# Optimization experiments

Measured on AMD Instinct MI355X. Metric: run time of the kernel, lower is better.

## Reference

```python
import jax, jax.numpy as jnp
import numpy as np

B, S, H, D = 8, 1024, 8, 64      # batch, seq_len, num_heads, num_hidden
DM = H * D                        # input model dim = 512
DK = 64.0                         # d_k scale
EPS = 1e-3                        # keras GroupNormalization default epsilon


def setup_inputs() -> dict:
    key = jax.random.key(0)
    ks = jax.random.split(key, 12)
    sc = 1.0 / np.sqrt(DM)
    return {
        "query":  jax.random.normal(ks[0], (B, S, DM), jnp.float32),
        "key":    jax.random.normal(ks[1], (B, S, DM), jnp.float32),
        "values": jax.random.normal(ks[2], (B, S, DM), jnp.float32),
        "Wq": jax.random.normal(ks[3], (DM, 3 * H * D), jnp.float32) * sc,
        "bq": jnp.zeros((3 * H * D,), jnp.float32),
        "Wk": jax.random.normal(ks[4], (DM, 2 * H * D), jnp.float32) * sc,
        "bk": jnp.zeros((2 * H * D,), jnp.float32),
        "Wv": jax.random.normal(ks[5], (DM, H * D), jnp.float32) * sc,
        "bv": jnp.zeros((H * D,), jnp.float32),
        "gamma": jnp.ones((D,), jnp.float32),
        "beta": jnp.zeros((D,), jnp.float32),
        "lam": jax.random.uniform(ks[6], (1,), jnp.float32),          # trainable lambda
        "lambda_init": jax.random.uniform(ks[7], (1,), jnp.float32),  # frozen lambda_init
    }


def reference(query, key, values, Wq, bq, Wk, bk, Wv, bv, gamma, beta, lam, lambda_init):
    # projections -> (B, H, S, *)
    q = (query @ Wq + bq).reshape(B, S, H, 3 * D).transpose(0, 2, 1, 3)
    k = (key @ Wk + bk).reshape(B, S, H, 2 * D).transpose(0, 2, 1, 3)
    v = (values @ Wv + bv).reshape(B, S, H, D).transpose(0, 2, 1, 3)

    q1, q2, gate = jnp.split(q, 3, axis=-1)      # each (B,H,S,D)
    k1, k2 = k[..., :D], k[..., D:]

    inv = 1.0 / jnp.sqrt(jnp.float32(DK))
    s1 = jnp.einsum("bhqd,bhkd->bhqk", q1, k1) * inv
    s2 = jnp.einsum("bhqd,bhkd->bhqk", q2, k2) * inv

    # differential attention: dual softmax combined with learned lambda
    attn = jax.nn.softmax(s1, axis=-1) - lam[0] * jax.nn.softmax(s2, axis=-1)
    out = jnp.einsum("bhqk,bhkd->bhqd", attn, v)      # (B,H,S,D)
    out = out.transpose(0, 2, 1, 3)                    # (B,S,H,D)

    # keras GroupNormalization(groups=H, axis=-1) on channels D:
    # reshape channel dim into (groups, D//H), reduce over all non-batch,
    # non-group axes: (S, H, D//H)
    g = out.reshape(B, S, H, H, D // H)
    mean = jnp.mean(g, axis=(1, 2, 4), keepdims=True)
    var = jnp.var(g, axis=(1, 2, 4), keepdims=True)
    g = (g - mean) * jax.lax.rsqrt(var + EPS)
    out = g.reshape(B, S, H, D) * gamma + beta

    out = out * (1.0 - lambda_init[0])
    out = out * jax.nn.sigmoid(gate.transpose(0, 2, 1, 3))
    return out.reshape(B, S, H * D)
```

## Files before the change

kernel.cpp:

```cpp
#include <hip/hip_runtime.h>
#include <cstdint>
#include <cstddef>

#define B_ 8
#define S_ 1024
#define H_ 8
#define D_ 64
#define DM_ 512

typedef __bf16 bf16x8 __attribute__((ext_vector_type(8)));
typedef float floatx4 __attribute__((ext_vector_type(4)));
typedef unsigned short ushort8 __attribute__((ext_vector_type(8)));
typedef unsigned short ushort4v __attribute__((ext_vector_type(4)));

union Frag { ushort8 us; bf16x8 bf; };

#define MFMA(a, b, c) __builtin_amdgcn_mfma_f32_16x16x32_bf16((a), (b), (c), 0, 0, 0)

__device__ __forceinline__ unsigned short f2bf(float f) {
  unsigned int u = __float_as_uint(f);
  unsigned int r = (u + 0x7fffu + ((u >> 16) & 1u)) >> 16;
  return (unsigned short)r;
}

__device__ __forceinline__ void gload16(const void* g, void* l) {
  __builtin_amdgcn_global_load_lds(
      (const __attribute__((address_space(1))) unsigned int*)g,
      (__attribute__((address_space(3))) unsigned int*)l, 16, 0, 0);
}

__global__ __launch_bounds__(256) void cast_in(
    const float* __restrict__ q, const float* __restrict__ k,
    const float* __restrict__ v, unsigned short* __restrict__ abf)
{
  size_t i4 = ((size_t)blockIdx.x * 256 + threadIdx.x) * 4;
  const size_t SEG = (size_t)4 << 20;
  const float* src = (i4 < SEG) ? (q + i4)
                   : (i4 < 2 * SEG) ? (k + (i4 - SEG))
                                    : (v + (i4 - 2 * SEG));
  floatx4 f = *(const floatx4*)src;
  ushort4v o;
  o[0] = f2bf(f[0]); o[1] = f2bf(f[1]); o[2] = f2bf(f[2]); o[3] = f2bf(f[3]);
  *(ushort4v*)(abf + i4) = o;
}

__global__ __launch_bounds__(256) void wtrans(
    const float* __restrict__ Wq, const float* __restrict__ Wk,
    const float* __restrict__ Wv, unsigned short* __restrict__ wt)
{
  const int tid = threadIdx.x;
  const int k0 = blockIdx.x * 64;
  const int n0 = blockIdx.y * 64;
  const float* src; int ncols, nb;
  if (n0 < 1536)      { src = Wq; ncols = 1536; nb = n0; }
  else if (n0 < 2560) { src = Wk; ncols = 1024; nb = n0 - 1536; }
  else                { src = Wv; ncols = 512;  nb = n0 - 2560; }

  __shared__ unsigned short sT[64][72];
  const int kr0 = tid >> 4, nc4 = (tid & 15) * 4;
  #pragma unroll
  for (int i = 0; i < 4; i++) {
    int kr = kr0 + i * 16;
    floatx4 f = *(const floatx4*)(src + (size_t)(k0 + kr) * ncols + nb + nc4);
    sT[nc4 + 0][kr] = f2bf(f[0]);
    sT[nc4 + 1][kr] = f2bf(f[1]);
    sT[nc4 + 2][kr] = f2bf(f[2]);
    sT[nc4 + 3][kr] = f2bf(f[3]);
  }
  __syncthreads();
  const int nr0 = tid >> 3, kc8 = (tid & 7) * 8;
  #pragma unroll
  for (int i = 0; i < 2; i++) {
    int nr = nr0 + i * 32;
    *(ushort8*)(wt + (size_t)(n0 + nr) * 512 + k0 + kc8) = *(const ushort8*)&sT[nr][kc8];
  }
}

__global__ __launch_bounds__(256) void gemm_kernel(
    const unsigned short* __restrict__ abf, const unsigned short* __restrict__ wt,
    const float* __restrict__ bq, const float* __restrict__ bk,
    const float* __restrict__ bv,
    unsigned short* __restrict__ q1, unsigned short* __restrict__ q2,
    float* __restrict__ gate, unsigned short* __restrict__ k1,
    unsigned short* __restrict__ k2, unsigned short* __restrict__ vT)
{
  const int tid  = threadIdx.x;
  const int wave = tid >> 6;
  const int lane = tid & 63;
  const int l16  = lane & 15;
  const int quad = lane >> 4;
  const int mt = blockIdx.x;
  const int nt = blockIdx.y;
  const int wm = wave & 1, wn = wave >> 1;

  const unsigned short* Asrc =
      abf + (nt < 12 ? 0 : nt < 20 ? ((size_t)4 << 20) : ((size_t)8 << 20));

  __shared__ unsigned short sMem[2 * 128 * 64];
  unsigned short* sA = sMem;
  unsigned short* sB = sMem + 128 * 64;

  floatx4 acc[4][4];
  #pragma unroll
  for (int i = 0; i < 4; i++)
    #pragma unroll
    for (int j = 0; j < 4; j++)
      #pragma unroll
      for (int r = 0; r < 4; r++) acc[i][j][r] = 0.0f;

  const int lrow   = lane >> 3;
  const int lchunk = lane & 7;
  const int gchunk = lchunk ^ lrow;
  const int rkey   = l16 & 7;

  for (int kt = 0; kt < 8; kt++) {
    #pragma unroll
    for (int j = 0; j < 4; j++) {
      int r8 = (wave * 4 + j) * 8;
      gload16(Asrc + (size_t)(mt * 128 + r8 + lrow) * 512 + kt * 64 + gchunk * 8,
              &sA[(wave * 4 + j) * 512]);
      gload16(wt + (size_t)(nt * 128 + r8 + lrow) * 512 + kt * 64 + gchunk * 8,
              &sB[(wave * 4 + j) * 512]);
    }
    __syncthreads();
    #pragma unroll
    for (int c = 0; c < 2; c++) {
      Frag af[4], bf[4];
      #pragma unroll
      for (int mi = 0; mi < 4; mi++)
        af[mi].us = *(const ushort8*)&sA[(wm * 64 + mi * 16 + l16) * 64 +
                                         (((c * 4 + quad) ^ rkey) << 3)];
      #pragma unroll
      for (int ni = 0; ni < 4; ni++)
        bf[ni].us = *(const ushort8*)&sB[(wn * 64 + ni * 16 + l16) * 64 +
                                         (((c * 4 + quad) ^ rkey) << 3)];
      #pragma unroll
      for (int mi = 0; mi < 4; mi++)
        #pragma unroll
        for (int ni = 0; ni < 4; ni++)
          acc[mi][ni] = MFMA(af[mi].bf, bf[ni].bf, acc[mi][ni]);
    }
    __syncthreads();
  }

  const int gm0 = mt * 128 + wm * 64;
  const int bb  = gm0 >> 10;
  const int s0  = gm0 & 1023;
  const int nseg = nt * 2 + wn;
  unsigned short* sC = sMem + wave * 4096;

  int h, sel = 0; bool isV = false;
  const float* bias_arr; int nb0;
  unsigned short* dstb = nullptr;
  if (nseg < 24)      { h = nseg / 3; sel = nseg % 3; bias_arr = bq; nb0 = nseg * 64;
                        dstb = (sel == 0) ? q1 : (sel == 1) ? q2 : nullptr; }
  else if (nseg < 40) { int t = nseg - 24; h = t >> 1; sel = t & 1;
                        bias_arr = bk; nb0 = t * 64; dstb = sel ? k2 : k1; }
  else                { h = nseg - 40; isV = true; bias_arr = bv; nb0 = (nseg - 40) * 64; }

  if (dstb != nullptr || isV) {
    #pragma unroll
    for (int ni = 0; ni < 4; ni++) {
      float bv_ = bias_arr[nb0 + ni * 16 + l16];
      #pragma unroll
      for (int mi = 0; mi < 4; mi++)
        #pragma unroll
        for (int r = 0; r < 4; r++) {
          float val = acc[mi][ni][r] + bv_;
          int ml = mi * 16 + quad * 4 + r;
          int nl = ni * 16 + l16;
          if (!isV) {
            int ch = (nl >> 3) ^ (ml & 7);
            sC[ml * 64 + (ch << 3) + (nl & 7)] = f2bf(val);
          } else {
            int ch = (ml >> 3) ^ (nl & 7);
            sC[nl * 64 + (ch << 3) + (ml & 7)] = f2bf(val);
          }
        }
    }
    const int rr = lane >> 3, cc = lane & 7;
    if (!isV) {
      unsigned short* base = dstb + ((size_t)(bb * H_ + h) * S_ + s0) * D_;
      #pragma unroll
      for (int j = 0; j < 8; j++) {
        int row = j * 8 + rr;
        int logc = cc ^ (row & 7);
        ushort8 valv = *(const ushort8*)&sC[row * 64 + cc * 8];
        *(ushort8*)(base + (size_t)row * D_ + logc * 8) = valv;
      }
    } else {
      unsigned short* base = vT + ((size_t)(bb * H_ + h) * D_) * S_ + s0;
      #pragma unroll
      for (int j = 0; j < 8; j++) {
        int drow = j * 8 + rr;
        int logc = cc ^ (drow & 7);
        ushort8 valv = *(const ushort8*)&sC[drow * 64 + cc * 8];
        *(ushort8*)(base + (size_t)drow * S_ + logc * 8) = valv;
      }
    }
  } else {
    #pragma unroll
    for (int ni = 0; ni < 4; ni++) {
      float bv_ = bias_arr[nb0 + ni * 16 + l16];
      #pragma unroll
      for (int mi = 0; mi < 4; mi++)
        #pragma unroll
        for (int r = 0; r < 4; r++) {
          int s = s0 + mi * 16 + quad * 4 + r;
          int d = ni * 16 + l16;
          gate[((size_t)(bb * H_ + h) * S_ + s) * D_ + d] = acc[mi][ni][r] + bv_;
        }
    }
  }
}

__global__ __launch_bounds__(256, 4) void attn_kernel(
    const unsigned short* __restrict__ q1, const unsigned short* __restrict__ q2,
    const unsigned short* __restrict__ k1, const unsigned short* __restrict__ k2,
    const unsigned short* __restrict__ vT, const float* __restrict__ lamp,
    float* __restrict__ O)
{
  const int tid  = threadIdx.x;
  const int wave = tid >> 6;
  const int lane = tid & 63;
  const int l16  = lane & 15;
  const int quad = lane >> 4;
  const int bh = blockIdx.x & 63;
  const int qt = blockIdx.x >> 6;

  __shared__ unsigned short sK1[64][72];
  __shared__ unsigned short sK2[64][72];
  __shared__ unsigned short sVt[64][72];
  __shared__ unsigned short sP[64][72];

  const int q0 = qt * 64;
  const size_t qoff = ((size_t)bh * S_ + q0 + wave * 16 + l16) * D_;
  Frag qf1[2], qf2[2];
  #pragma unroll
  for (int c = 0; c < 2; c++) {
    qf1[c].us = *(const ushort8*)(q1 + qoff + c * 32 + quad * 8);
    qf2[c].us = *(const ushort8*)(q2 + qoff + c * 32 + quad * 8);
  }

  floatx4 o1[4], o2[4];
  float l1[4], l2[4];
  #pragma unroll
  for (int i = 0; i < 4; i++) {
    #pragma unroll
    for (int j = 0; j < 4; j++) { o1[i][j] = 0.f; o2[i][j] = 0.f; }
    l1[i] = 0.f; l2[i] = 0.f;
  }

  const unsigned short* kb1 = k1 + (size_t)bh * S_ * D_;
  const unsigned short* kb2 = k2 + (size_t)bh * S_ * D_;
  const unsigned short* vb  = vT + (size_t)bh * D_ * S_;

  const int prow = wave * 16 + quad * 4;
  const int pq   = (l16 >> 2) & 3;

  for (int kt = 0; kt < 16; kt++) {
    __syncthreads();
    #pragma unroll
    for (int i = 0; i < 2; i++) {
      int idx = tid + i * 256;
      int r = idx >> 3, c8 = (idx & 7) * 8;
      *(ushort8*)&sK1[r][c8] = *(const ushort8*)(kb1 + (size_t)(kt * 64 + r) * 64 + c8);
      *(ushort8*)&sK2[r][c8] = *(const ushort8*)(kb2 + (size_t)(kt * 64 + r) * 64 + c8);
      *(ushort8*)&sVt[r][c8] = *(const ushort8*)(vb + (size_t)r * S_ + kt * 64 + c8);
    }
    __syncthreads();

    {
      floatx4 s[4];
      #pragma unroll
      for (int nt = 0; nt < 4; nt++)
        #pragma unroll
        for (int j = 0; j < 4; j++) s[nt][j] = 0.f;
      #pragma unroll
      for (int c = 0; c < 2; c++)
        #pragma unroll
        for (int nt = 0; nt < 4; nt++) {
          Frag kf; kf.us = *(const ushort8*)&sK1[nt * 16 + l16][c * 32 + quad * 8];
          s[nt] = MFMA(qf1[c].bf, kf.bf, s[nt]);
        }
      #pragma unroll
      for (int nt = 0; nt < 4; nt++)
        #pragma unroll
        for (int r = 0; r < 4; r++) {
          float p = __expf(s[nt][r] * 0.125f);
          l1[r] += p;
          sP[prow + r][((nt ^ quad) << 4) + l16] = f2bf(p);
        }
      #pragma unroll
      for (int c = 0; c < 2; c++) {
        int pg = (c * 2 + (quad >> 1)) ^ pq;
        Frag pa; pa.us = *(const ushort8*)&sP[wave * 16 + l16][pg * 16 + (quad & 1) * 8];
        #pragma unroll
        for (int dt = 0; dt < 4; dt++) {
          Frag vf; vf.us = *(const ushort8*)&sVt[dt * 16 + l16][c * 32 + quad * 8];
          o1[dt] = MFMA(pa.bf, vf.bf, o1[dt]);
        }
      }
    }
    {
      floatx4 s[4];
      #pragma unroll
      for (int nt = 0; nt < 4; nt++)
        #pragma unroll
        for (int j = 0; j < 4; j++) s[nt][j] = 0.f;
      #pragma unroll
      for (int c = 0; c < 2; c++)
        #pragma unroll
        for (int nt = 0; nt < 4; nt++) {
          Frag kf; kf.us = *(const ushort8*)&sK2[nt * 16 + l16][c * 32 + quad * 8];
          s[nt] = MFMA(qf2[c].bf, kf.bf, s[nt]);
        }
      #pragma unroll
      for (int nt = 0; nt < 4; nt++)
        #pragma unroll
        for (int r = 0; r < 4; r++) {
          float p = __expf(s[nt][r] * 0.125f);
          l2[r] += p;
          sP[prow + r][((nt ^ quad) << 4) + l16] = f2bf(p);
        }
      #pragma unroll
      for (int c = 0; c < 2; c++) {
        int pg = (c * 2 + (quad >> 1)) ^ pq;
        Frag pa; pa.us = *(const ushort8*)&sP[wave * 16 + l16][pg * 16 + (quad & 1) * 8];
        #pragma unroll
        for (int dt = 0; dt < 4; dt++) {
          Frag vf; vf.us = *(const ushort8*)&sVt[dt * 16 + l16][c * 32 + quad * 8];
          o2[dt] = MFMA(pa.bf, vf.bf, o2[dt]);
        }
      }
    }
  }

  #pragma unroll
  for (int r = 0; r < 4; r++) {
    #pragma unroll
    for (int off = 1; off < 16; off <<= 1) {
      l1[r] += __shfl_xor(l1[r], off);
      l2[r] += __shfl_xor(l2[r], off);
    }
  }

  const float lam = lamp[0];
  #pragma unroll
  for (int r = 0; r < 4; r++) {
    float i1 = 1.0f / l1[r], i2 = lam / l2[r];
    int row = q0 + wave * 16 + quad * 4 + r;
    #pragma unroll
    for (int dt = 0; dt < 4; dt++) {
      O[((size_t)bh * S_ + row) * D_ + dt * 16 + l16] = o1[dt][r] * i1 - o2[dt][r] * i2;
    }
  }
}

__global__ __launch_bounds__(256) void stats1(const float* __restrict__ O,
                                              float* __restrict__ partial)
{
  const int g = blockIdx.x >> 2, ch = blockIdx.x & 3;
  const int b = g >> 3, j = g & 7;
  const float* base = O + (size_t)b * 8 * 65536;
  float s = 0.f, s2 = 0.f;
  for (int t = threadIdx.x; t < 16384; t += 256) {
    int hh = t >> 11;
    int ss = ch * 256 + ((t >> 3) & 255);
    int r  = t & 7;
    float x = base[(size_t)hh * 65536 + ss * 64 + j * 8 + r];
    s += x; s2 += x * x;
  }
  #pragma unroll
  for (int m = 32; m; m >>= 1) { s += __shfl_down(s, m); s2 += __shfl_down(s2, m); }
  __shared__ float red[8];
  if ((threadIdx.x & 63) == 0) {
    red[(threadIdx.x >> 6) * 2]     = s;
    red[(threadIdx.x >> 6) * 2 + 1] = s2;
  }
  __syncthreads();
  if (threadIdx.x == 0) {
    float S1 = 0.f, S2 = 0.f;
    #pragma unroll
    for (int w = 0; w < 4; w++) { S1 += red[w * 2]; S2 += red[w * 2 + 1]; }
    partial[blockIdx.x * 2]     = S1;
    partial[blockIdx.x * 2 + 1] = S2;
  }
}

__global__ __launch_bounds__(64) void stats2(const float* __restrict__ partial,
                                             float* __restrict__ stats)
{
  int g = threadIdx.x;
  float S1 = 0.f, S2 = 0.f;
  #pragma unroll
  for (int ch = 0; ch < 4; ch++) {
    S1 += partial[(g * 4 + ch) * 2];
    S2 += partial[(g * 4 + ch) * 2 + 1];
  }
  float mean = S1 / 65536.f;
  float var  = S2 / 65536.f - mean * mean;
  stats[g]      = mean;
  stats[64 + g] = rsqrtf(var + 0.001f);
}

__global__ __launch_bounds__(256) void final_kernel(
    const float* __restrict__ O, const float* __restrict__ gate,
    const float* __restrict__ stats, const float* __restrict__ gamma,
    const float* __restrict__ beta, const float* __restrict__ li,
    float* __restrict__ out)
{
  int e = blockIdx.x * 256 + threadIdx.x;
  int d  = e & 63;
  int hh = (e >> 6) & 7;
  int s  = (e >> 9) & 1023;
  int b  = e >> 19;
  size_t oidx = (size_t)(b * 8 + hh) * 65536 + (size_t)s * 64 + d;
  int g = b * 8 + (d >> 3);
  float x = (O[oidx] - stats[g]) * stats[64 + g];
  x = x * gamma[d] + beta[d];
  x *= (1.0f - li[0]);
  float gt = gate[oidx];
  x *= 1.0f / (1.0f + __expf(-gt));
  out[e] = x;
}

extern "C" void kernel_launch(void* const* d_in, const int* in_sizes, int n_in,
                              void* d_out, int out_size, void* d_ws, size_t ws_size,
                              hipStream_t stream)
{
  const float* query  = (const float*)d_in[0];
  const float* key    = (const float*)d_in[1];
  const float* values = (const float*)d_in[2];
  const float* Wq = (const float*)d_in[3];
  const float* bq = (const float*)d_in[4];
  const float* Wk = (const float*)d_in[5];
  const float* bk = (const float*)d_in[6];
  const float* Wv = (const float*)d_in[7];
  const float* bv = (const float*)d_in[8];
  const float* gamma = (const float*)d_in[9];
  const float* beta  = (const float*)d_in[10];
  const float* lam   = (const float*)d_in[11];
  const float* lami  = (const float*)d_in[12];
  float* out = (float*)d_out;

  char* ws = (char*)d_ws;
  const size_t MB = (size_t)1 << 20;
  unsigned short* abf = (unsigned short*)(ws);
  float*          O   = (float*)(ws);
  unsigned short* wt  = (unsigned short*)(ws + 24 * MB);
  float* partial      = (float*)(ws + 27 * MB);
  float* stats        = (float*)(ws + 27 * MB + 65536);
  unsigned short* q1  = (unsigned short*)(ws + 28 * MB);
  unsigned short* q2  = (unsigned short*)(ws + 36 * MB);
  unsigned short* k1  = (unsigned short*)(ws + 44 * MB);
  unsigned short* k2  = (unsigned short*)(ws + 52 * MB);
  unsigned short* vT  = (unsigned short*)(ws + 60 * MB);
  float* gate         = (float*)(ws + 68 * MB);

  cast_in<<<12288, 256, 0, stream>>>(query, key, values, abf);
  wtrans<<<dim3(8, 48), 256, 0, stream>>>(Wq, Wk, Wv, wt);
  gemm_kernel<<<dim3(64, 24), 256, 0, stream>>>(abf, wt, bq, bk, bv,
                                                q1, q2, gate, k1, k2, vT);
  attn_kernel<<<dim3(1024), 256, 0, stream>>>(q1, q2, k1, k2, vT, lam, O);
  stats1<<<256, 256, 0, stream>>>(O, partial);
  stats2<<<1, 64, 0, stream>>>(partial, stats);
  final_kernel<<<16384, 256, 0, stream>>>(O, gate, stats, gamma, beta, lami, out);
}
```

Before: 252.7 us.

## Use direct global-to-LDS loads with XOR swizzle in attention and merge small kernels

The attention kernel now loads K1, K2 and V^T tiles with global_load_lds into an unpadded, XOR-swizzled LDS layout instead of staging through registers. It also uses exp2f with a prescaled constant in place of __expf. The cast and weight-transpose kernels become one launch, and the stats2 kernel is removed: final_kernel now reduces the partial sums per element. This cuts launch count and register-staged copies, but every thread of final_kernel now repeats the partial-sum reads, and the loop now relies on a trailing barrier for correctness.

```diff
diff --git a/kernel.cpp b/kernel.cpp
--- a/kernel.cpp
+++ b/kernel.cpp
@@ -29,34 +29,34 @@
       (__attribute__((address_space(3))) unsigned int*)l, 16, 0, 0);
 }
 
-__global__ __launch_bounds__(256) void cast_in(
+__global__ __launch_bounds__(256) void prep_kernel(
     const float* __restrict__ q, const float* __restrict__ k,
-    const float* __restrict__ v, unsigned short* __restrict__ abf)
-{
-  size_t i4 = ((size_t)blockIdx.x * 256 + threadIdx.x) * 4;
-  const size_t SEG = (size_t)4 << 20;
-  const float* src = (i4 < SEG) ? (q + i4)
-                   : (i4 < 2 * SEG) ? (k + (i4 - SEG))
-                                    : (v + (i4 - 2 * SEG));
-  floatx4 f = *(const floatx4*)src;
-  ushort4v o;
-  o[0] = f2bf(f[0]); o[1] = f2bf(f[1]); o[2] = f2bf(f[2]); o[3] = f2bf(f[3]);
-  *(ushort4v*)(abf + i4) = o;
-}
-
-__global__ __launch_bounds__(256) void wtrans(
+    const float* __restrict__ v, unsigned short* __restrict__ abf,
     const float* __restrict__ Wq, const float* __restrict__ Wk,
     const float* __restrict__ Wv, unsigned short* __restrict__ wt)
 {
+  __shared__ unsigned short sT[64][72];
   const int tid = threadIdx.x;
-  const int k0 = blockIdx.x * 64;
-  const int n0 = blockIdx.y * 64;
+  if (blockIdx.x < 12288) {
+    size_t i4 = ((size_t)blockIdx.x * 256 + tid) * 4;
+    const size_t SEG = (size_t)4 << 20;
+    const float* src = (i4 < SEG) ? (q + i4)
+                     : (i4 < 2 * SEG) ? (k + (i4 - SEG))
+                                      : (v + (i4 - 2 * SEG));
+    floatx4 f = *(const floatx4*)src;
+    ushort4v o;
+    o[0] = f2bf(f[0]); o[1] = f2bf(f[1]); o[2] = f2bf(f[2]); o[3] = f2bf(f[3]);
+    *(ushort4v*)(abf + i4) = o;
+    return;
+  }
+  const int bid = blockIdx.x - 12288;
+  const int k0 = (bid & 7) * 64;
+  const int n0 = (bid >> 3) * 64;
   const float* src; int ncols, nb;
   if (n0 < 1536)      { src = Wq; ncols = 1536; nb = n0; }
   else if (n0 < 2560) { src = Wk; ncols = 1024; nb = n0 - 1536; }
   else                { src = Wv; ncols = 512;  nb = n0 - 2560; }
 
-  __shared__ unsigned short sT[64][72];
   const int kr0 = tid >> 4, nc4 = (tid & 15) * 4;
   #pragma unroll
   for (int i = 0; i < 4; i++) {
@@ -228,10 +228,10 @@
   const int bh = blockIdx.x & 63;
   const int qt = blockIdx.x >> 6;
 
-  __shared__ unsigned short sK1[64][72];
-  __shared__ unsigned short sK2[64][72];
-  __shared__ unsigned short sVt[64][72];
-  __shared__ unsigned short sP[64][72];
+  __shared__ unsigned short sK1[64 * 64];
+  __shared__ unsigned short sK2[64 * 64];
+  __shared__ unsigned short sVt[64 * 64];
+  __shared__ unsigned short sP [64 * 72];
 
   const int q0 = qt * 64;
   const size_t qoff = ((size_t)bh * S_ + q0 + wave * 16 + l16) * D_;
@@ -255,18 +255,20 @@
   const unsigned short* kb2 = k2 + (size_t)bh * S_ * D_;
   const unsigned short* vb  = vT + (size_t)bh * D_ * S_;
 
+  const int srow = lane >> 3;
+  const int sgch = (lane & 7) ^ srow;
+  const int rkey = l16 & 7;
   const int prow = wave * 16 + quad * 4;
   const int pq   = (l16 >> 2) & 3;
+  const float SCL = 0.18033688011f;
 
   for (int kt = 0; kt < 16; kt++) {
-    __syncthreads();
     #pragma unroll
     for (int i = 0; i < 2; i++) {
-      int idx = tid + i * 256;
-      int r = idx >> 3, c8 = (idx & 7) * 8;
-      *(ushort8*)&sK1[r][c8] = *(const ushort8*)(kb1 + (size_t)(kt * 64 + r) * 64 + c8);
-      *(ushort8*)&sK2[r][c8] = *(const ushort8*)(kb2 + (size_t)(kt * 64 + r) * 64 + c8);
-      *(ushort8*)&sVt[r][c8] = *(const ushort8*)(vb + (size_t)r * S_ + kt * 64 + c8);
+      int r0 = wave * 16 + i * 8;
+      gload16(kb1 + (size_t)(kt * 64 + r0 + srow) * 64 + sgch * 8, &sK1[r0 * 64]);
+      gload16(kb2 + (size_t)(kt * 64 + r0 + srow) * 64 + sgch * 8, &sK2[r0 * 64]);
+      gload16(vb  + (size_t)(r0 + srow) * S_ + kt * 64 + sgch * 8, &sVt[r0 * 64]);
     }
     __syncthreads();
 
@@ -280,24 +282,27 @@
       for (int c = 0; c < 2; c++)
         #pragma unroll
         for (int nt = 0; nt < 4; nt++) {
-          Frag kf; kf.us = *(const ushort8*)&sK1[nt * 16 + l16][c * 32 + quad * 8];
+          Frag kf; kf.us = *(const ushort8*)&sK1[(nt * 16 + l16) * 64 +
+                                                 (((c * 4 + quad) ^ rkey) << 3)];
           s[nt] = MFMA(qf1[c].bf, kf.bf, s[nt]);
         }
       #pragma unroll
       for (int nt = 0; nt < 4; nt++)
         #pragma unroll
         for (int r = 0; r < 4; r++) {
-          float p = __expf(s[nt][r] * 0.125f);
+          float p = exp2f(s[nt][r] * SCL);
           l1[r] += p;
-          sP[prow + r][((nt ^ quad) << 4) + l16] = f2bf(p);
+          sP[(prow + r) * 72 + ((nt ^ quad) << 4) + l16] = f2bf(p);
         }
       #pragma unroll
       for (int c = 0; c < 2; c++) {
         int pg = (c * 2 + (quad >> 1)) ^ pq;
-        Frag pa; pa.us = *(const ushort8*)&sP[wave * 16 + l16][pg * 16 + (quad & 1) * 8];
+        Frag pa; pa.us = *(const ushort8*)&sP[(wave * 16 + l16) * 72 +
+                                              pg * 16 + (quad & 1) * 8];
         #pragma unroll
         for (int dt = 0; dt < 4; dt++) {
-          Frag vf; vf.us = *(const ushort8*)&sVt[dt * 16 + l16][c * 32 + quad * 8];
+          Frag vf; vf.us = *(const ushort8*)&sVt[(dt * 16 + l16) * 64 +
+                                                 (((c * 4 + quad) ^ rkey) << 3)];
           o1[dt] = MFMA(pa.bf, vf.bf, o1[dt]);
         }
       }
@@ -312,28 +317,32 @@
       for (int c = 0; c < 2; c++)
         #pragma unroll
         for (int nt = 0; nt < 4; nt++) {
-          Frag kf; kf.us = *(const ushort8*)&sK2[nt * 16 + l16][c * 32 + quad * 8];
+          Frag kf; kf.us = *(const ushort8*)&sK2[(nt * 16 + l16) * 64 +
+                                                 (((c * 4 + quad) ^ rkey) << 3)];
           s[nt] = MFMA(qf2[c].bf, kf.bf, s[nt]);
         }
       #pragma unroll
       for (int nt = 0; nt < 4; nt++)
         #pragma unroll
         for (int r = 0; r < 4; r++) {
-          float p = __expf(s[nt][r] * 0.125f);
+          float p = exp2f(s[nt][r] * SCL);
           l2[r] += p;
-          sP[prow + r][((nt ^ quad) << 4) + l16] = f2bf(p);
+          sP[(prow + r) * 72 + ((nt ^ quad) << 4) + l16] = f2bf(p);
         }
       #pragma unroll
       for (int c = 0; c < 2; c++) {
         int pg = (c * 2 + (quad >> 1)) ^ pq;
-        Frag pa; pa.us = *(const ushort8*)&sP[wave * 16 + l16][pg * 16 + (quad & 1) * 8];
+        Frag pa; pa.us = *(const ushort8*)&sP[(wave * 16 + l16) * 72 +
+                                              pg * 16 + (quad & 1) * 8];
         #pragma unroll
         for (int dt = 0; dt < 4; dt++) {
-          Frag vf; vf.us = *(const ushort8*)&sVt[dt * 16 + l16][c * 32 + quad * 8];
+          Frag vf; vf.us = *(const ushort8*)&sVt[(dt * 16 + l16) * 64 +
+                                                 (((c * 4 + quad) ^ rkey) << 3)];
           o2[dt] = MFMA(pa.bf, vf.bf, o2[dt]);
         }
       }
     }
+    __syncthreads();
   }
 
   #pragma unroll
@@ -388,25 +397,9 @@
   }
 }
 
-__global__ __launch_bounds__(64) void stats2(const float* __restrict__ partial,
-                                             float* __restrict__ stats)
-{
-  int g = threadIdx.x;
-  float S1 = 0.f, S2 = 0.f;
-  #pragma unroll
-  for (int ch = 0; ch < 4; ch++) {
-    S1 += partial[(g * 4 + ch) * 2];
-    S2 += partial[(g * 4 + ch) * 2 + 1];
-  }
-  float mean = S1 / 65536.f;
-  float var  = S2 / 65536.f - mean * mean;
-  stats[g]      = mean;
-  stats[64 + g] = rsqrtf(var + 0.001f);
-}
-
 __global__ __launch_bounds__(256) void final_kernel(
     const float* __restrict__ O, const float* __restrict__ gate,
-    const float* __restrict__ stats, const float* __restrict__ gamma,
+    const float* __restrict__ partial, const float* __restrict__ gamma,
     const float* __restrict__ beta, const float* __restrict__ li,
     float* __restrict__ out)
 {
@@ -417,7 +410,15 @@
   int b  = e >> 19;
   size_t oidx = (size_t)(b * 8 + hh) * 65536 + (size_t)s * 64 + d;
   int g = b * 8 + (d >> 3);
-  float x = (O[oidx] - stats[g]) * stats[64 + g];
+  float S1 = 0.f, S2 = 0.f;
+  #pragma unroll
+  for (int ch = 0; ch < 4; ch++) {
+    S1 += partial[(g * 4 + ch) * 2];
+    S2 += partial[(g * 4 + ch) * 2 + 1];
+  }
+  float mean = S1 * (1.0f / 65536.f);
+  float inv  = rsqrtf(S2 * (1.0f / 65536.f) - mean * mean + 0.001f);
+  float x = (O[oidx] - mean) * inv;
   x = x * gamma[d] + beta[d];
   x *= (1.0f - li[0]);
   float gt = gate[oidx];
@@ -450,7 +451,6 @@
   float*          O   = (float*)(ws);
   unsigned short* wt  = (unsigned short*)(ws + 24 * MB);
   float* partial      = (float*)(ws + 27 * MB);
-  float* stats        = (float*)(ws + 27 * MB + 65536);
   unsigned short* q1  = (unsigned short*)(ws + 28 * MB);
   unsigned short* q2  = (unsigned short*)(ws + 36 * MB);
   unsigned short* k1  = (unsigned short*)(ws + 44 * MB);
@@ -458,12 +458,10 @@
   unsigned short* vT  = (unsigned short*)(ws + 60 * MB);
   float* gate         = (float*)(ws + 68 * MB);
 
-  cast_in<<<12288, 256, 0, stream>>>(query, key, values, abf);
-  wtrans<<<dim3(8, 48), 256, 0, stream>>>(Wq, Wk, Wv, wt);
+  prep_kernel<<<12672, 256, 0, stream>>>(query, key, values, abf, Wq, Wk, Wv, wt);
   gemm_kernel<<<dim3(64, 24), 256, 0, stream>>>(abf, wt, bq, bk, bv,
                                                 q1, q2, gate, k1, k2, vT);
   attn_kernel<<<dim3(1024), 256, 0, stream>>>(q1, q2, k1, k2, vT, lam, O);
   stats1<<<256, 256, 0, stream>>>(O, partial);
-  stats2<<<1, 64, 0, stream>>>(partial, stats);
-  final_kernel<<<16384, 256, 0, stream>>>(O, gate, stats, gamma, beta, lami, out);
-}
+  final_kernel<<<16384, 256, 0, stream>>>(O, gate, partial, gamma, beta, lami, out);
+}
```

After: 268.8 us. 6.4% more time.
